# Optimization experiments

Measured on AMD Instinct MI355X. Metric: run time of the kernel, lower is better.

The kernel has to match this reference:

```python
import jax, jax.numpy as jnp
import numpy as np

N_NODES = 100000
N_EDGES = 1600000
NEG_SLOPE = 0.2  # DGL GATConv default leaky_relu slope
BN_EPS = 1e-5


def setup_inputs() -> dict:
    key = jax.random.key(0)
    ks = jax.random.split(key, 10)
    feats = jax.random.normal(ks[0], (N_NODES, 128), dtype=jnp.float32)
    src = jax.random.randint(ks[1], (N_EDGES,), 0, N_NODES, dtype=jnp.int64)
    dst = jax.random.randint(ks[2], (N_EDGES,), 0, N_NODES, dtype=jnp.int64)
    fc_w = jax.random.normal(ks[3], (256, 128), dtype=jnp.float32) * 0.05   # H*D x in_feats
    attn_l = jax.random.normal(ks[4], (4, 64), dtype=jnp.float32) * 0.05
    attn_r = jax.random.normal(ks[5], (4, 64), dtype=jnp.float32) * 0.05
    res_w = jax.random.normal(ks[6], (256, 128), dtype=jnp.float32) * 0.05  # residual projection
    bias = jax.random.normal(ks[7], (4, 64), dtype=jnp.float32) * 0.05
    gamma = jnp.ones((64,), dtype=jnp.float32)
    beta = jnp.zeros((64,), dtype=jnp.float32)
    return {"feats": feats, "src": src, "dst": dst, "fc_w": fc_w,
            "attn_l": attn_l, "attn_r": attn_r, "res_w": res_w,
            "bias": bias, "gamma": gamma, "beta": beta}


def reference(feats, src, dst, fc_w, attn_l, attn_r, res_w, bias, gamma, beta):
    N = feats.shape[0]
    H, D = attn_l.shape
    # projected features [N, H, D] (feat_drop is identity in eval mode)
    h = (feats @ fc_w.T).reshape(N, H, D)
    # per-node attention logits [N, H]
    el = jnp.sum(h * attn_l[None], axis=-1)
    er = jnp.sum(h * attn_r[None], axis=-1)
    # edge logits, leaky relu
    e = el[src] + er[dst]                       # [E, H]
    e = jnp.where(e > 0, e, NEG_SLOPE * e)
    # numerically stable segment softmax over incoming edges of each dst node
    m = jax.ops.segment_max(e, dst, num_segments=N)       # [N, H]
    ex = jnp.exp(e - m[dst])                               # [E, H]
    s = jax.ops.segment_sum(ex, dst, num_segments=N)       # [N, H]
    alpha = ex / s[dst]                                    # [E, H]
    # weighted message aggregation: scatter-add alpha * h_src into dst
    msg = h[src] * alpha[:, :, None]                       # [E, H, D]
    rst = jax.ops.segment_sum(msg, dst, num_segments=N)    # [N, H, D]
    # residual projection + bias + activation (elu)
    res = (feats @ res_w.T).reshape(N, H, D)
    rst = jax.nn.elu(rst + res + bias[None])
    # mean over heads -> [N, D]
    out = rst.mean(axis=1)
    # BatchNorm1d (training stats: biased variance over the node/batch axis)
    mu = out.mean(axis=0)
    var = out.var(axis=0)
    return (out - mu) * jax.lax.rsqrt(var + BN_EPS) * gamma + beta
```

## Files before the change

### kernel.cpp

```cpp
#include <hip/hip_runtime.h>

#define N_NODES 100000
#define N_EDGES 1600000
#define NEG_SLOPE 0.2f
#define BN_EPS 1e-5f

typedef __attribute__((ext_vector_type(8))) short short8;
typedef __attribute__((ext_vector_type(4))) float floatx4;

static const size_t OFF_AB   = 0;
static const size_t OFF_BB   = 25624576;
static const size_t OFF_H    = 25755648;
static const size_t OFF_RES  = 76956672;
static const size_t OFF_EL   = 128156672;
static const size_t OFF_ER   = 129757184;
static const size_t OFF_DEG  = 131357184;
static const size_t OFF_RS   = 131757184;
static const size_t OFF_CUR  = 132157568;
static const size_t OFF_ESRC = 132557568;
static const size_t OFF_BS   = 142157568;
static const size_t OFF_BN   = 142158080;

__device__ __forceinline__ unsigned short f2bf(float x) {
  unsigned int u = __float_as_uint(x);
  unsigned int r = (u + 0x7fffu + ((u >> 16) & 1u)) >> 16;
  return (unsigned short)r;
}
__device__ __forceinline__ float bf2f(unsigned short u) {
  return __uint_as_float(((unsigned int)u) << 16);
}

__global__ __launch_bounds__(256) void k_pre(
    const float* __restrict__ feats, const float* __restrict__ fc_w,
    const float* __restrict__ res_w, const int* __restrict__ dst,
    unsigned short* __restrict__ Ab, unsigned short* __restrict__ Bb,
    int* __restrict__ deg, unsigned short* __restrict__ hbuf,
    float* __restrict__ el)
{
  const int b = blockIdx.x;
  if (b < 6256) {
    int c = b * 256 + threadIdx.x;
    int r = c >> 4, j = c & 15;
    unsigned short v[8];
    if (r < N_NODES) {
      const float* p = feats + (size_t)r * 128 + j * 8;
      float4 a = *(const float4*)p, bb = *(const float4*)(p + 4);
      v[0]=f2bf(a.x); v[1]=f2bf(a.y); v[2]=f2bf(a.z); v[3]=f2bf(a.w);
      v[4]=f2bf(bb.x); v[5]=f2bf(bb.y); v[6]=f2bf(bb.z); v[7]=f2bf(bb.w);
    } else {
      for (int i = 0; i < 8; i++) v[i] = 0;
    }
    size_t idx = (size_t)(r >> 7) * 2048 + ((r >> 4) & 7) * 256 + (j >> 2) * 64
               + (r & 15) + 16 * (j & 3);
    *(short8*)(Ab + idx * 8) = *(short8*)v;
  } else if (b < 12506) {
    int e = (b - 6256) * 256 + threadIdx.x;
    if (e < N_EDGES) atomicAdd(&deg[dst[e]], 1);
  } else if (b < 12538) {
    int c = (b - 12506) * 256 + threadIdx.x;
    int n = c >> 4, j = c & 15;
    const float* W = (n < 256) ? (fc_w + (size_t)n * 128) : (res_w + (size_t)(n - 256) * 128);
    const float* p = W + j * 8;
    float4 a = *(const float4*)p, bb = *(const float4*)(p + 4);
    unsigned short v[8];
    v[0]=f2bf(a.x); v[1]=f2bf(a.y); v[2]=f2bf(a.z); v[3]=f2bf(a.w);
    v[4]=f2bf(bb.x); v[5]=f2bf(bb.y); v[6]=f2bf(bb.z); v[7]=f2bf(bb.w);
    size_t idx = (size_t)(n >> 7) * 2048 + ((n >> 4) & 7) * 256 + (j >> 2) * 64
               + (n & 15) + 16 * (j & 3);
    *(short8*)(Bb + idx * 8) = *(short8*)v;
  } else {
    const int t = threadIdx.x;
    hbuf[(size_t)N_NODES * 256 + t] = 0;
    if (t < 4) el[N_NODES * 4 + t] = -1e30f;
  }
}

__global__ __launch_bounds__(256) void k_mm(
    const unsigned short* __restrict__ Ab, const unsigned short* __restrict__ Bb,
    const float* __restrict__ bias, const float* __restrict__ attn_l,
    const float* __restrict__ attn_r,
    unsigned short* __restrict__ hbuf, unsigned short* __restrict__ resbuf,
    float* __restrict__ el, float* __restrict__ er)
{
  __shared__ unsigned short sA[16384];
  const int tid = threadIdx.x;
  const int w = tid >> 6, L = tid & 63;
  const int blk = blockIdx.x, nb = blockIdx.y;

  {
    const unsigned short* ga = Ab + (size_t)blk * 16384;
    #pragma unroll
    for (int i = 0; i < 8; i++) {
      int off = (i * 256 + w * 64) * 8;
      __builtin_amdgcn_global_load_lds(
          (const __attribute__((address_space(1))) unsigned int*)(ga + off + L * 8),
          (__attribute__((address_space(3))) unsigned int*)(sA + off),
          16, 0, 0);
    }
  }
  const int mh = w & 1, nh = w >> 1;
  floatx4 acc[4][4] = {};
  __syncthreads();

  const unsigned short* gb = Bb + ((size_t)nb * 2048 + nh * 4 * 256) * 8 + L * 8;
  #pragma unroll
  for (int s = 0; s < 4; s++) {
    short8 a[4], b[4];
    #pragma unroll
    for (int t = 0; t < 4; t++)
      a[t] = *(const short8*)(sA + ((mh * 4 + t) * 256 + s * 64 + L) * 8);
    #pragma unroll
    for (int t = 0; t < 4; t++)
      b[t] = *(const short8*)(gb + ((size_t)t * 256 + s * 64) * 8);
    #pragma unroll
    for (int mt = 0; mt < 4; mt++)
      #pragma unroll
      for (int nt = 0; nt < 4; nt++)
        acc[mt][nt] = __builtin_amdgcn_mfma_f32_16x16x32_bf16(a[mt], b[nt], acc[mt][nt], 0, 0, 0);
  }

  const int q = L >> 4, cn = L & 15;
  const int r0 = blk * 128 + mh * 64;
  if (nb < 2) {
    const int head = nb * 2 + nh;
    const int col0 = nb * 128 + nh * 64;
    float al[4], ar[4];
    #pragma unroll
    for (int nt = 0; nt < 4; nt++) {
      al[nt] = attn_l[head * 64 + nt * 16 + cn];
      ar[nt] = attn_r[head * 64 + nt * 16 + cn];
    }
    #pragma unroll
    for (int mt = 0; mt < 4; mt++)
      #pragma unroll
      for (int r = 0; r < 4; r++) {
        const int row = r0 + mt * 16 + q * 4 + r;
        float pl = 0.f, pr = 0.f;
        #pragma unroll
        for (int nt = 0; nt < 4; nt++) {
          pl = fmaf(acc[mt][nt][r], al[nt], pl);
          pr = fmaf(acc[mt][nt][r], ar[nt], pr);
        }
        #pragma unroll
        for (int o = 1; o < 16; o <<= 1) {
          pl += __shfl_xor(pl, o, 64);
          pr += __shfl_xor(pr, o, 64);
        }
        if (row < N_NODES) {
          #pragma unroll
          for (int nt = 0; nt < 4; nt++)
            hbuf[(size_t)row * 256 + col0 + nt * 16 + cn] = f2bf(acc[mt][nt][r]);
          if (cn == 0) {
            el[row * 4 + head] = pl;
            er[row * 4 + head] = pr;
          }
        }
      }
  } else {
    const int rc0 = (nb - 2) * 128 + nh * 64;
    #pragma unroll
    for (int mt = 0; mt < 4; mt++)
      #pragma unroll
      for (int r = 0; r < 4; r++) {
        const int row = r0 + mt * 16 + q * 4 + r;
        if (row < N_NODES)
          #pragma unroll
          for (int nt = 0; nt < 4; nt++) {
            float v = acc[mt][nt][r] + bias[rc0 + nt * 16 + cn];
            resbuf[(size_t)row * 256 + rc0 + nt * 16 + cn] = f2bf(v);
          }
      }
  }
}

__global__ __launch_bounds__(256) void k_scan1(const int* __restrict__ deg,
                                               int* __restrict__ rs, int* __restrict__ bsums)
{
  __shared__ int tmp[256];
  const int t = threadIdx.x;
  const int base = blockIdx.x * 1024 + t * 4;
  int v0 = 0, v1 = 0, v2 = 0, v3 = 0;
  if (base + 0 < N_NODES) v0 = (deg[base + 0] + 3) & ~3;
  if (base + 1 < N_NODES) v1 = (deg[base + 1] + 3) & ~3;
  if (base + 2 < N_NODES) v2 = (deg[base + 2] + 3) & ~3;
  if (base + 3 < N_NODES) v3 = (deg[base + 3] + 3) & ~3;
  const int tsum = v0 + v1 + v2 + v3;
  tmp[t] = tsum;
  __syncthreads();
  for (int o = 1; o < 256; o <<= 1) {
    int x = (t >= o) ? tmp[t - o] : 0;
    __syncthreads();
    tmp[t] += x;
    __syncthreads();
  }
  const int excl = tmp[t] - tsum;
  if (base + 0 < N_NODES) rs[base + 0] = excl;
  if (base + 1 < N_NODES) rs[base + 1] = excl + v0;
  if (base + 2 < N_NODES) rs[base + 2] = excl + v0 + v1;
  if (base + 3 < N_NODES) rs[base + 3] = excl + v0 + v1 + v2;
  if (t == 255) bsums[blockIdx.x] = tmp[t];
}

__global__ __launch_bounds__(256) void k_scan3(int* __restrict__ rs,
                                               const int* __restrict__ bsums,
                                               int* __restrict__ cursor,
                                               const int* __restrict__ deg,
                                               int* __restrict__ esrc)
{
  __shared__ int sb[128];
  const int t = threadIdx.x;
  int raw = 0;
  if (t < 128) { raw = (t < 98) ? bsums[t] : 0; sb[t] = raw; }
  __syncthreads();
  for (int o = 1; o < 128; o <<= 1) {
    int x = (t >= o && t < 128) ? sb[t - o] : 0;
    __syncthreads();
    if (t < 128) sb[t] += x;
    __syncthreads();
  }
  if (t < 128) sb[t] -= raw;
  __syncthreads();
  const int i = blockIdx.x * 256 + t;
  if (i < N_NODES) {
    int v = rs[i] + sb[i >> 10];
    rs[i] = v;
    cursor[i] = v;
    const int d = deg[i];
    const int pd = (d + 3) & ~3;
    for (int j = d; j < pd; j++) esrc[v + j] = N_NODES;
    if (i == N_NODES - 1) rs[N_NODES] = v + pd;
  }
}

__global__ __launch_bounds__(256) void k_scatter(const int* __restrict__ src,
                                                 const int* __restrict__ dst,
                                                 int* __restrict__ cursor,
                                                 int* __restrict__ esrc)
{
  int e = blockIdx.x * 256 + threadIdx.x;
  if (e >= N_EDGES) return;
  int d = dst[e];
  int pos = atomicAdd(&cursor[d], 1);
  esrc[pos] = src[e];
}

#define RFL(x) __builtin_amdgcn_readfirstlane(x)

#define LOADSN4(SN, PP) do { SN = *(const int4*)(esrc + (PP)); } while (0)

#define GATHER4(EV, HV, SN) do { \
  const int g0_ = RFL(SN.x), g1_ = RFL(SN.y), g2_ = RFL(SN.z), g3_ = RFL(SN.w); \
  HV##0 = *(const ushort4*)(hbuf + (size_t)g0_ * 256 + lane4); \
  HV##1 = *(const ushort4*)(hbuf + (size_t)g1_ * 256 + lane4); \
  HV##2 = *(const ushort4*)(hbuf + (size_t)g2_ * 256 + lane4); \
  HV##3 = *(const ushort4*)(hbuf + (size_t)g3_ * 256 + lane4); \
  EV##0 = el[g0_ * 4 + head]; \
  EV##1 = el[g1_ * 4 + head]; \
  EV##2 = el[g2_ * 4 + head]; \
  EV##3 = el[g3_ * 4 + head]; \
} while (0)

#define EDGE1(EVi, HVi) do { \
  float e_ = EVi + ern; \
  e_ = (e_ > 0.f) ? e_ : NEG_SLOPE * e_; \
  const float w_ = __expf(e_); \
  ssum += w_; \
  acc.x = fmaf(w_, bf2f(HVi.x), acc.x); \
  acc.y = fmaf(w_, bf2f(HVi.y), acc.y); \
  acc.z = fmaf(w_, bf2f(HVi.z), acc.z); \
  acc.w = fmaf(w_, bf2f(HVi.w), acc.w); \
} while (0)

#define COMPUTE4(EV, HV) do { \
  EDGE1(EV##0, HV##0); EDGE1(EV##1, HV##1); \
  EDGE1(EV##2, HV##2); EDGE1(EV##3, HV##3); \
} while (0)

#define FIN(ND) do { \
  const float inv_ = (ssum > 0.f) ? (1.0f / ssum) : 0.f; \
  float vx_ = fmaf(acc.x, inv_, bf2f(rv_cur.x)); \
  float vy_ = fmaf(acc.y, inv_, bf2f(rv_cur.y)); \
  float vz_ = fmaf(acc.z, inv_, bf2f(rv_cur.z)); \
  float vw_ = fmaf(acc.w, inv_, bf2f(rv_cur.w)); \
  vx_ = (vx_ > 0.f) ? vx_ : (__expf(vx_) - 1.f); \
  vy_ = (vy_ > 0.f) ? vy_ : (__expf(vy_) - 1.f); \
  vz_ = (vz_ > 0.f) ? vz_ : (__expf(vz_) - 1.f); \
  vw_ = (vw_ > 0.f) ? vw_ : (__expf(vw_) - 1.f); \
  vx_ += __shfl_xor(vx_, 16, 64); vx_ += __shfl_xor(vx_, 32, 64); \
  vy_ += __shfl_xor(vy_, 16, 64); vy_ += __shfl_xor(vy_, 32, 64); \
  vz_ += __shfl_xor(vz_, 16, 64); vz_ += __shfl_xor(vz_, 32, 64); \
  vw_ += __shfl_xor(vw_, 16, 64); vw_ += __shfl_xor(vw_, 32, 64); \
  if (lane < 16) { \
    float4 o_; \
    o_.x = vx_ * 0.25f; o_.y = vy_ * 0.25f; o_.z = vz_ * 0.25f; o_.w = vw_ * 0.25f; \
    *(float4*)(out + (size_t)(ND) * 64 + lane4) = o_; \
  } \
} while (0)

#define BOUNDARY() \
  while (p == nend) { \
    FIN(nu); \
    acc.x = 0.f; acc.y = 0.f; acc.z = 0.f; acc.w = 0.f; ssum = 0.f; \
    nu++; \
    nend = nendN; ern = ernN; rv_cur = rvN; \
    const int f1_ = (nu + 1 < N_NODES) ? (nu + 1) : (N_NODES - 1); \
    const int f2_ = (nu + 2 <= N_NODES) ? (nu + 2) : N_NODES; \
    nendN = RFL(rs[f2_]); \
    ernN = er[f1_ * 4 + head]; \
    rvN = *(const ushort4*)(resbuf + (size_t)f1_ * 256 + lane4); \
  }

__global__ __launch_bounds__(256, 4) void k_agg(
    const unsigned short* __restrict__ hbuf, const unsigned short* __restrict__ resbuf,
    const float* __restrict__ el, const float* __restrict__ er,
    const int* __restrict__ rs, const int* __restrict__ esrc,
    float* __restrict__ out)
{
  const int lane = threadIdx.x & 63;
  const int head = lane >> 4;
  const int lane4 = lane * 4;
  const int wid = blockIdx.x * 4 + (threadIdx.x >> 6);
  const int nW = gridDim.x * 4;

  const int n0 = (int)(((long long)wid * N_NODES) / nW);
  const int n1 = (int)(((long long)(wid + 1) * N_NODES) / nW);
  if (n0 >= n1) return;

  int nu = RFL(n0);
  const int p_end = RFL(rs[n1]);
  int nend = RFL(rs[nu + 1]);
  {
  }
  int f1 = (nu + 1 < N_NODES) ? (nu + 1) : (N_NODES - 1);
  int f2 = (nu + 2 <= N_NODES) ? (nu + 2) : N_NODES;
  int nendN = RFL(rs[f2]);
  float ern  = er[nu * 4 + head];
  float ernN = er[f1 * 4 + head];
  ushort4 rv_cur = *(const ushort4*)(resbuf + (size_t)nu * 256 + lane4);
  ushort4 rvN    = *(const ushort4*)(resbuf + (size_t)f1 * 256 + lane4);

  float4 acc = make_float4(0.f, 0.f, 0.f, 0.f);
  float ssum = 0.f;

  int4 snA, snB, snC, snD;
  float evA0, evA1, evA2, evA3, evB0, evB1, evB2, evB3;
  float evC0, evC1, evC2, evC3, evD0, evD1, evD2, evD3;
  ushort4 hvA0, hvA1, hvA2, hvA3, hvB0, hvB1, hvB2, hvB3;
  ushort4 hvC0, hvC1, hvC2, hvC3, hvD0, hvD1, hvD2, hvD3;

  int p = RFL(rs[nu]);
  if (p      < p_end) { LOADSN4(snA, p);      GATHER4(evA, hvA, snA); }
  if (p + 4  < p_end) { LOADSN4(snB, p + 4);  GATHER4(evB, hvB, snB); }
  if (p + 8  < p_end) { LOADSN4(snC, p + 8);  GATHER4(evC, hvC, snC); }
  if (p + 12 < p_end) { LOADSN4(snD, p + 12); }

  while (p < p_end) {
    if (p + 12 < p_end) GATHER4(evD, hvD, snD);
    if (p + 16 < p_end) LOADSN4(snA, p + 16);
    BOUNDARY();
    COMPUTE4(evA, hvA);
    p += 4; if (p >= p_end) break;
    if (p + 12 < p_end) GATHER4(evA, hvA, snA);
    if (p + 16 < p_end) LOADSN4(snB, p + 16);
    BOUNDARY();
    COMPUTE4(evB, hvB);
    p += 4; if (p >= p_end) break;
    if (p + 12 < p_end) GATHER4(evB, hvB, snB);
    if (p + 16 < p_end) LOADSN4(snC, p + 16);
    BOUNDARY();
    COMPUTE4(evC, hvC);
    p += 4; if (p >= p_end) break;
    if (p + 12 < p_end) GATHER4(evC, hvC, snC);
    if (p + 16 < p_end) LOADSN4(snD, p + 16);
    BOUNDARY();
    COMPUTE4(evD, hvD);
    p += 4;
  }

  while (nu < n1) {
    FIN(nu);
    acc.x = 0.f; acc.y = 0.f; acc.z = 0.f; acc.w = 0.f; ssum = 0.f;
    nu++;
    if (nu < n1) rv_cur = *(const ushort4*)(resbuf + (size_t)nu * 256 + lane4);
  }
}

__global__ __launch_bounds__(256) void k_bn_stats(const float* __restrict__ out,
                                                  float* __restrict__ bn)
{
  const int t = threadIdx.x;
  const int c4 = (t & 15) * 4;
  const int rg = t >> 4;
  float4 s = make_float4(0.f, 0.f, 0.f, 0.f);
  float4 q = make_float4(0.f, 0.f, 0.f, 0.f);
  for (int row = blockIdx.x * 16 + rg; row < N_NODES; row += gridDim.x * 16) {
    float4 v = *(const float4*)(out + (size_t)row * 64 + c4);
    s.x += v.x; s.y += v.y; s.z += v.z; s.w += v.w;
    q.x += v.x * v.x; q.y += v.y * v.y; q.z += v.z * v.z; q.w += v.w * v.w;
  }
  __shared__ float ls[64], lq[64];
  if (t < 64) { ls[t] = 0.f; lq[t] = 0.f; }
  __syncthreads();
  atomicAdd(&ls[c4 + 0], s.x); atomicAdd(&ls[c4 + 1], s.y);
  atomicAdd(&ls[c4 + 2], s.z); atomicAdd(&ls[c4 + 3], s.w);
  atomicAdd(&lq[c4 + 0], q.x); atomicAdd(&lq[c4 + 1], q.y);
  atomicAdd(&lq[c4 + 2], q.z); atomicAdd(&lq[c4 + 3], q.w);
  __syncthreads();
  if (t < 64) {
    atomicAdd(&bn[t], ls[t]);
    atomicAdd(&bn[64 + t], lq[t]);
  }
}

__global__ __launch_bounds__(256) void k_bn_apply(float* __restrict__ out,
                                                  const float* __restrict__ bn,
                                                  const float* __restrict__ gamma,
                                                  const float* __restrict__ beta)
{
  __shared__ float sc[64], sh[64];
  const int t = threadIdx.x;
  if (t < 64) {
    float mean = bn[t] * (1.0f / N_NODES);
    float var = bn[64 + t] * (1.0f / N_NODES) - mean * mean;
    float s = gamma[t] * rsqrtf(var + BN_EPS);
    sc[t] = s;
    sh[t] = beta[t] - mean * s;
  }
  __syncthreads();
  const int i = blockIdx.x * 256 + t;
  if (i >= N_NODES * 16) return;
  const int d0 = (i & 15) * 4;
  float4 v = *(float4*)(out + (size_t)i * 4);
  v.x = fmaf(v.x, sc[d0 + 0], sh[d0 + 0]);
  v.y = fmaf(v.y, sc[d0 + 1], sh[d0 + 1]);
  v.z = fmaf(v.z, sc[d0 + 2], sh[d0 + 2]);
  v.w = fmaf(v.w, sc[d0 + 3], sh[d0 + 3]);
  *(float4*)(out + (size_t)i * 4) = v;
}

extern "C" void kernel_launch(void* const* d_in, const int* in_sizes, int n_in,
                              void* d_out, int out_size, void* d_ws, size_t ws_size,
                              hipStream_t stream)
{
  const float* feats  = (const float*)d_in[0];
  const int*   src    = (const int*)d_in[1];
  const int*   dst    = (const int*)d_in[2];
  const float* fc_w   = (const float*)d_in[3];
  const float* attn_l = (const float*)d_in[4];
  const float* attn_r = (const float*)d_in[5];
  const float* res_w  = (const float*)d_in[6];
  const float* bias   = (const float*)d_in[7];
  const float* gamma  = (const float*)d_in[8];
  const float* beta   = (const float*)d_in[9];

  char* ws = (char*)d_ws;
  unsigned short* Ab     = (unsigned short*)(ws + OFF_AB);
  unsigned short* Bb     = (unsigned short*)(ws + OFF_BB);
  unsigned short* hbuf   = (unsigned short*)(ws + OFF_H);
  unsigned short* resbuf = (unsigned short*)(ws + OFF_RES);
  float* elb    = (float*)(ws + OFF_EL);
  float* erb    = (float*)(ws + OFF_ER);
  int*   deg    = (int*)(ws + OFF_DEG);
  int*   rsb    = (int*)(ws + OFF_RS);
  int*   curb   = (int*)(ws + OFF_CUR);
  int*   esrc   = (int*)(ws + OFF_ESRC);
  int*   bsums  = (int*)(ws + OFF_BS);
  float* bnb    = (float*)(ws + OFF_BN);
  float* outp   = (float*)d_out;

  hipMemsetAsync(deg, 0, N_NODES * sizeof(int), stream);
  hipMemsetAsync(bnb, 0, 128 * sizeof(float), stream);

  k_pre<<<12539, 256, 0, stream>>>(feats, fc_w, res_w, dst, Ab, Bb, deg, hbuf, elb);
  k_mm<<<dim3(782, 4), 256, 0, stream>>>(Ab, Bb, bias, attn_l, attn_r,
                                         hbuf, resbuf, elb, erb);
  k_scan1<<<98, 256, 0, stream>>>(deg, rsb, bsums);
  k_scan3<<<391, 256, 0, stream>>>(rsb, bsums, curb, deg, esrc);
  k_scatter<<<6250, 256, 0, stream>>>(src, dst, curb, esrc);
  k_agg<<<2048, 256, 0, stream>>>(hbuf, resbuf, elb, erb, rsb, esrc, outp);
  k_bn_stats<<<256, 256, 0, stream>>>(outp, bnb);
  k_bn_apply<<<6250, 256, 0, stream>>>(outp, bnb, gamma, beta);
}
```

Baseline: 515.9 us.

## Reuse A tile across two N-blocks in matmul; split edges across half-waves in aggregation

The matmul kernel now loads each A tile into LDS once and loops over two N-blocks, halving the grid's y dimension and the repeated A traffic. The aggregation kernel changes from one wave handling four edges per step with 4 features per lane to each half-wave processing a different edge with 8 features per lane via 16-byte loads. Partial sums are combined across halves with cross-lane shuffles at node boundaries. This is meant to increase per-lane load width and memory-level parallelism, at the cost of extra shuffles, a phase-aligned prologue, and fewer matmul blocks.

```diff
diff --git a/kernel.cpp b/kernel.cpp
--- a/kernel.cpp
+++ b/kernel.cpp
@@ -7,6 +7,7 @@
 
 typedef __attribute__((ext_vector_type(8))) short short8;
 typedef __attribute__((ext_vector_type(4))) float floatx4;
+typedef __attribute__((ext_vector_type(8))) unsigned short u16x8;
 
 static const size_t OFF_AB   = 0;
 static const size_t OFF_BB   = 25624576;
@@ -85,7 +86,7 @@
   __shared__ unsigned short sA[16384];
   const int tid = threadIdx.x;
   const int w = tid >> 6, L = tid & 63;
-  const int blk = blockIdx.x, nb = blockIdx.y;
+  const int blk = blockIdx.x;
 
   {
     const unsigned short* ga = Ab + (size_t)blk * 16384;
@@ -99,77 +100,80 @@
     }
   }
   const int mh = w & 1, nh = w >> 1;
-  floatx4 acc[4][4] = {};
-  __syncthreads();
-
-  const unsigned short* gb = Bb + ((size_t)nb * 2048 + nh * 4 * 256) * 8 + L * 8;
-  #pragma unroll
-  for (int s = 0; s < 4; s++) {
-    short8 a[4], b[4];
+  __syncthreads();
+
+  for (int wb = 0; wb < 2; ++wb) {
+    const int nb = blockIdx.y + wb * 2;
+    floatx4 acc[4][4] = {};
+    const unsigned short* gb = Bb + ((size_t)nb * 2048 + nh * 4 * 256) * 8 + L * 8;
     #pragma unroll
-    for (int t = 0; t < 4; t++)
-      a[t] = *(const short8*)(sA + ((mh * 4 + t) * 256 + s * 64 + L) * 8);
-    #pragma unroll
-    for (int t = 0; t < 4; t++)
-      b[t] = *(const short8*)(gb + ((size_t)t * 256 + s * 64) * 8);
-    #pragma unroll
-    for (int mt = 0; mt < 4; mt++)
+    for (int s = 0; s < 4; s++) {
+      short8 a[4], b[4];
       #pragma unroll
-      for (int nt = 0; nt < 4; nt++)
-        acc[mt][nt] = __builtin_amdgcn_mfma_f32_16x16x32_bf16(a[mt], b[nt], acc[mt][nt], 0, 0, 0);
-  }
-
-  const int q = L >> 4, cn = L & 15;
-  const int r0 = blk * 128 + mh * 64;
-  if (nb < 2) {
-    const int head = nb * 2 + nh;
-    const int col0 = nb * 128 + nh * 64;
-    float al[4], ar[4];
-    #pragma unroll
-    for (int nt = 0; nt < 4; nt++) {
-      al[nt] = attn_l[head * 64 + nt * 16 + cn];
-      ar[nt] = attn_r[head * 64 + nt * 16 + cn];
+      for (int t = 0; t < 4; t++)
+        a[t] = *(const short8*)(sA + ((mh * 4 + t) * 256 + s * 64 + L) * 8);
+      #pragma unroll
+      for (int t = 0; t < 4; t++)
+        b[t] = *(const short8*)(gb + ((size_t)t * 256 + s * 64) * 8);
+      #pragma unroll
+      for (int mt = 0; mt < 4; mt++)
+        #pragma unroll
+        for (int nt = 0; nt < 4; nt++)
+          acc[mt][nt] = __builtin_amdgcn_mfma_f32_16x16x32_bf16(a[mt], b[nt], acc[mt][nt], 0, 0, 0);
     }
-    #pragma unroll
-    for (int mt = 0; mt < 4; mt++)
+
+    const int q = L >> 4, cn = L & 15;
+    const int r0 = blk * 128 + mh * 64;
+    if (nb < 2) {
+      const int head = nb * 2 + nh;
+      const int col0 = nb * 128 + nh * 64;
+      float al[4], ar[4];
       #pragma unroll
-      for (int r = 0; r < 4; r++) {
-        const int row = r0 + mt * 16 + q * 4 + r;
-        float pl = 0.f, pr = 0.f;
+      for (int nt = 0; nt < 4; nt++) {
+        al[nt] = attn_l[head * 64 + nt * 16 + cn];
+        ar[nt] = attn_r[head * 64 + nt * 16 + cn];
+      }
+      #pragma unroll
+      for (int mt = 0; mt < 4; mt++)
         #pragma unroll
-        for (int nt = 0; nt < 4; nt++) {
-          pl = fmaf(acc[mt][nt][r], al[nt], pl);
-          pr = fmaf(acc[mt][nt][r], ar[nt], pr);
-        }
-        #pragma unroll
-        for (int o = 1; o < 16; o <<= 1) {
-          pl += __shfl_xor(pl, o, 64);
-          pr += __shfl_xor(pr, o, 64);
-        }
-        if (row < N_NODES) {
+        for (int r = 0; r < 4; r++) {
+          const int row = r0 + mt * 16 + q * 4 + r;
+          float pl = 0.f, pr = 0.f;
           #pragma unroll
-          for (int nt = 0; nt < 4; nt++)
-            hbuf[(size_t)row * 256 + col0 + nt * 16 + cn] = f2bf(acc[mt][nt][r]);
-          if (cn == 0) {
-            el[row * 4 + head] = pl;
-            er[row * 4 + head] = pr;
+          for (int nt = 0; nt < 4; nt++) {
+            pl = fmaf(acc[mt][nt][r], al[nt], pl);
+            pr = fmaf(acc[mt][nt][r], ar[nt], pr);
+          }
+          #pragma unroll
+          for (int o = 1; o < 16; o <<= 1) {
+            pl += __shfl_xor(pl, o, 64);
+            pr += __shfl_xor(pr, o, 64);
+          }
+          if (row < N_NODES) {
+            #pragma unroll
+            for (int nt = 0; nt < 4; nt++)
+              hbuf[(size_t)row * 256 + col0 + nt * 16 + cn] = f2bf(acc[mt][nt][r]);
+            if (cn == 0) {
+              el[row * 4 + head] = pl;
+              er[row * 4 + head] = pr;
+            }
           }
         }
-      }
-  } else {
-    const int rc0 = (nb - 2) * 128 + nh * 64;
-    #pragma unroll
-    for (int mt = 0; mt < 4; mt++)
+    } else {
+      const int rc0 = (nb - 2) * 128 + nh * 64;
       #pragma unroll
-      for (int r = 0; r < 4; r++) {
-        const int row = r0 + mt * 16 + q * 4 + r;
-        if (row < N_NODES)
-          #pragma unroll
-          for (int nt = 0; nt < 4; nt++) {
-            float v = acc[mt][nt][r] + bias[rc0 + nt * 16 + cn];
-            resbuf[(size_t)row * 256 + rc0 + nt * 16 + cn] = f2bf(v);
-          }
-      }
+      for (int mt = 0; mt < 4; mt++)
+        #pragma unroll
+        for (int r = 0; r < 4; r++) {
+          const int row = r0 + mt * 16 + q * 4 + r;
+          if (row < N_NODES)
+            #pragma unroll
+            for (int nt = 0; nt < 4; nt++) {
+              float v = acc[mt][nt][r] + bias[rc0 + nt * 16 + cn];
+              resbuf[(size_t)row * 256 + rc0 + nt * 16 + cn] = f2bf(v);
+            }
+        }
+    }
   }
 }
 
@@ -246,69 +250,95 @@
 
 #define RFL(x) __builtin_amdgcn_readfirstlane(x)
 
-#define LOADSN4(SN, PP) do { SN = *(const int4*)(esrc + (PP)); } while (0)
-
-#define GATHER4(EV, HV, SN) do { \
-  const int g0_ = RFL(SN.x), g1_ = RFL(SN.y), g2_ = RFL(SN.z), g3_ = RFL(SN.w); \
-  HV##0 = *(const ushort4*)(hbuf + (size_t)g0_ * 256 + lane4); \
-  HV##1 = *(const ushort4*)(hbuf + (size_t)g1_ * 256 + lane4); \
-  HV##2 = *(const ushort4*)(hbuf + (size_t)g2_ * 256 + lane4); \
-  HV##3 = *(const ushort4*)(hbuf + (size_t)g3_ * 256 + lane4); \
-  EV##0 = el[g0_ * 4 + head]; \
-  EV##1 = el[g1_ * 4 + head]; \
-  EV##2 = el[g2_ * 4 + head]; \
-  EV##3 = el[g3_ * 4 + head]; \
+#define GATHER(X) do { \
+  const int s_ = (lane & 32) ? sn##X.y : sn##X.x; \
+  hv##X = *(const u16x8*)(hbuf + (size_t)s_ * 256 + li8); \
+  ev##X = el[s_ * 4 + head]; \
 } while (0)
 
-#define EDGE1(EVi, HVi) do { \
-  float e_ = EVi + ern; \
-  e_ = (e_ > 0.f) ? e_ : NEG_SLOPE * e_; \
+#define PRO(X, B) do { \
+  if ((B) < p_end) { sn##X = *(const int2*)(esrc + (B)); GATHER(X); } \
+} while (0)
+
+#define COMPUTE(X) do { \
+  float e_ = ev##X + ern; \
+  e_ = fmaxf(e_, NEG_SLOPE * e_); \
   const float w_ = __expf(e_); \
   ssum += w_; \
-  acc.x = fmaf(w_, bf2f(HVi.x), acc.x); \
-  acc.y = fmaf(w_, bf2f(HVi.y), acc.y); \
-  acc.z = fmaf(w_, bf2f(HVi.z), acc.z); \
-  acc.w = fmaf(w_, bf2f(HVi.w), acc.w); \
+  accA.x = fmaf(w_, bf2f(hv##X[0]), accA.x); \
+  accA.y = fmaf(w_, bf2f(hv##X[1]), accA.y); \
+  accA.z = fmaf(w_, bf2f(hv##X[2]), accA.z); \
+  accA.w = fmaf(w_, bf2f(hv##X[3]), accA.w); \
+  accB.x = fmaf(w_, bf2f(hv##X[4]), accB.x); \
+  accB.y = fmaf(w_, bf2f(hv##X[5]), accB.y); \
+  accB.z = fmaf(w_, bf2f(hv##X[6]), accB.z); \
+  accB.w = fmaf(w_, bf2f(hv##X[7]), accB.w); \
 } while (0)
 
-#define COMPUTE4(EV, HV) do { \
-  EDGE1(EV##0, HV##0); EDGE1(EV##1, HV##1); \
-  EDGE1(EV##2, HV##2); EDGE1(EV##3, HV##3); \
-} while (0)
-
 #define FIN(ND) do { \
-  const float inv_ = (ssum > 0.f) ? (1.0f / ssum) : 0.f; \
-  float vx_ = fmaf(acc.x, inv_, bf2f(rv_cur.x)); \
-  float vy_ = fmaf(acc.y, inv_, bf2f(rv_cur.y)); \
-  float vz_ = fmaf(acc.z, inv_, bf2f(rv_cur.z)); \
-  float vw_ = fmaf(acc.w, inv_, bf2f(rv_cur.w)); \
-  vx_ = (vx_ > 0.f) ? vx_ : (__expf(vx_) - 1.f); \
-  vy_ = (vy_ > 0.f) ? vy_ : (__expf(vy_) - 1.f); \
-  vz_ = (vz_ > 0.f) ? vz_ : (__expf(vz_) - 1.f); \
-  vw_ = (vw_ > 0.f) ? vw_ : (__expf(vw_) - 1.f); \
-  vx_ += __shfl_xor(vx_, 16, 64); vx_ += __shfl_xor(vx_, 32, 64); \
-  vy_ += __shfl_xor(vy_, 16, 64); vy_ += __shfl_xor(vy_, 32, 64); \
-  vz_ += __shfl_xor(vz_, 16, 64); vz_ += __shfl_xor(vz_, 32, 64); \
-  vw_ += __shfl_xor(vw_, 16, 64); vw_ += __shfl_xor(vw_, 32, 64); \
-  if (lane < 16) { \
-    float4 o_; \
-    o_.x = vx_ * 0.25f; o_.y = vy_ * 0.25f; o_.z = vz_ * 0.25f; o_.w = vw_ * 0.25f; \
-    *(float4*)(out + (size_t)(ND) * 64 + lane4) = o_; \
+  float st_ = ssum + __shfl_xor(ssum, 32, 64); \
+  float a0_ = accA.x + __shfl_xor(accA.x, 32, 64); \
+  float a1_ = accA.y + __shfl_xor(accA.y, 32, 64); \
+  float a2_ = accA.z + __shfl_xor(accA.z, 32, 64); \
+  float a3_ = accA.w + __shfl_xor(accA.w, 32, 64); \
+  float a4_ = accB.x + __shfl_xor(accB.x, 32, 64); \
+  float a5_ = accB.y + __shfl_xor(accB.y, 32, 64); \
+  float a6_ = accB.z + __shfl_xor(accB.z, 32, 64); \
+  float a7_ = accB.w + __shfl_xor(accB.w, 32, 64); \
+  const float inv_ = (st_ > 0.f) ? (1.0f / st_) : 0.f; \
+  a0_ = fmaf(a0_, inv_, bf2f(rv_cur[0])); \
+  a1_ = fmaf(a1_, inv_, bf2f(rv_cur[1])); \
+  a2_ = fmaf(a2_, inv_, bf2f(rv_cur[2])); \
+  a3_ = fmaf(a3_, inv_, bf2f(rv_cur[3])); \
+  a4_ = fmaf(a4_, inv_, bf2f(rv_cur[4])); \
+  a5_ = fmaf(a5_, inv_, bf2f(rv_cur[5])); \
+  a6_ = fmaf(a6_, inv_, bf2f(rv_cur[6])); \
+  a7_ = fmaf(a7_, inv_, bf2f(rv_cur[7])); \
+  a0_ = (a0_ > 0.f) ? a0_ : (__expf(a0_) - 1.f); \
+  a1_ = (a1_ > 0.f) ? a1_ : (__expf(a1_) - 1.f); \
+  a2_ = (a2_ > 0.f) ? a2_ : (__expf(a2_) - 1.f); \
+  a3_ = (a3_ > 0.f) ? a3_ : (__expf(a3_) - 1.f); \
+  a4_ = (a4_ > 0.f) ? a4_ : (__expf(a4_) - 1.f); \
+  a5_ = (a5_ > 0.f) ? a5_ : (__expf(a5_) - 1.f); \
+  a6_ = (a6_ > 0.f) ? a6_ : (__expf(a6_) - 1.f); \
+  a7_ = (a7_ > 0.f) ? a7_ : (__expf(a7_) - 1.f); \
+  a0_ += __shfl_xor(a0_, 8, 64);  a0_ += __shfl_xor(a0_, 16, 64); \
+  a1_ += __shfl_xor(a1_, 8, 64);  a1_ += __shfl_xor(a1_, 16, 64); \
+  a2_ += __shfl_xor(a2_, 8, 64);  a2_ += __shfl_xor(a2_, 16, 64); \
+  a3_ += __shfl_xor(a3_, 8, 64);  a3_ += __shfl_xor(a3_, 16, 64); \
+  a4_ += __shfl_xor(a4_, 8, 64);  a4_ += __shfl_xor(a4_, 16, 64); \
+  a5_ += __shfl_xor(a5_, 8, 64);  a5_ += __shfl_xor(a5_, 16, 64); \
+  a6_ += __shfl_xor(a6_, 8, 64);  a6_ += __shfl_xor(a6_, 16, 64); \
+  a7_ += __shfl_xor(a7_, 8, 64);  a7_ += __shfl_xor(a7_, 16, 64); \
+  if (lane < 8) { \
+    float4 o1_, o2_; \
+    o1_.x = a0_ * 0.25f; o1_.y = a1_ * 0.25f; o1_.z = a2_ * 0.25f; o1_.w = a3_ * 0.25f; \
+    o2_.x = a4_ * 0.25f; o2_.y = a5_ * 0.25f; o2_.z = a6_ * 0.25f; o2_.w = a7_ * 0.25f; \
+    *(float4*)(out + (size_t)(ND) * 64 + li8) = o1_; \
+    *(float4*)(out + (size_t)(ND) * 64 + li8 + 4) = o2_; \
   } \
 } while (0)
 
 #define BOUNDARY() \
   while (p == nend) { \
     FIN(nu); \
-    acc.x = 0.f; acc.y = 0.f; acc.z = 0.f; acc.w = 0.f; ssum = 0.f; \
+    accA.x=0.f; accA.y=0.f; accA.z=0.f; accA.w=0.f; \
+    accB.x=0.f; accB.y=0.f; accB.z=0.f; accB.w=0.f; ssum = 0.f; \
     nu++; \
     nend = nendN; ern = ernN; rv_cur = rvN; \
     const int f1_ = (nu + 1 < N_NODES) ? (nu + 1) : (N_NODES - 1); \
     const int f2_ = (nu + 2 <= N_NODES) ? (nu + 2) : N_NODES; \
     nendN = RFL(rs[f2_]); \
     ernN = er[f1_ * 4 + head]; \
-    rvN = *(const ushort4*)(resbuf + (size_t)f1_ * 256 + lane4); \
-  }
+    rvN = *(const u16x8*)(resbuf + (size_t)f1_ * 256 + li8); \
+  }
+
+#define STEP(CUR, NXT) do { \
+  if (p + 6 < p_end) GATHER(NXT); \
+  if (p + 8 < p_end) sn##CUR = *(const int2*)(esrc + p + 8); \
+  BOUNDARY(); \
+  COMPUTE(CUR); \
+} while (0)
 
 __global__ __launch_bounds__(256, 4) void k_agg(
     const unsigned short* __restrict__ hbuf, const unsigned short* __restrict__ resbuf,
@@ -317,8 +347,9 @@
     float* __restrict__ out)
 {
   const int lane = threadIdx.x & 63;
-  const int head = lane >> 4;
-  const int lane4 = lane * 4;
+  const int li = lane & 31;
+  const int head = li >> 3;
+  const int li8 = li * 8;
   const int wid = blockIdx.x * 4 + (threadIdx.x >> 6);
   const int nW = gridDim.x * 4;
 
@@ -329,59 +360,49 @@
   int nu = RFL(n0);
   const int p_end = RFL(rs[n1]);
   int nend = RFL(rs[nu + 1]);
-  {
-  }
   int f1 = (nu + 1 < N_NODES) ? (nu + 1) : (N_NODES - 1);
   int f2 = (nu + 2 <= N_NODES) ? (nu + 2) : N_NODES;
   int nendN = RFL(rs[f2]);
   float ern  = er[nu * 4 + head];
   float ernN = er[f1 * 4 + head];
-  ushort4 rv_cur = *(const ushort4*)(resbuf + (size_t)nu * 256 + lane4);
-  ushort4 rvN    = *(const ushort4*)(resbuf + (size_t)f1 * 256 + lane4);
-
-  float4 acc = make_float4(0.f, 0.f, 0.f, 0.f);
+  u16x8 rv_cur = *(const u16x8*)(resbuf + (size_t)nu * 256 + li8);
+  u16x8 rvN    = *(const u16x8*)(resbuf + (size_t)f1 * 256 + li8);
+
+  float4 accA = make_float4(0.f, 0.f, 0.f, 0.f);
+  float4 accB = make_float4(0.f, 0.f, 0.f, 0.f);
   float ssum = 0.f;
 
-  int4 snA, snB, snC, snD;
-  float evA0, evA1, evA2, evA3, evB0, evB1, evB2, evB3;
-  float evC0, evC1, evC2, evC3, evD0, evD1, evD2, evD3;
-  ushort4 hvA0, hvA1, hvA2, hvA3, hvB0, hvB1, hvB2, hvB3;
-  ushort4 hvC0, hvC1, hvC2, hvC3, hvD0, hvD1, hvD2, hvD3;
+  int2 snA, snB, snC, snD;
+  float evA, evB, evC, evD;
+  u16x8 hvA, hvB, hvC, hvD;
 
   int p = RFL(rs[nu]);
-  if (p      < p_end) { LOADSN4(snA, p);      GATHER4(evA, hvA, snA); }
-  if (p + 4  < p_end) { LOADSN4(snB, p + 4);  GATHER4(evB, hvB, snB); }
-  if (p + 8  < p_end) { LOADSN4(snC, p + 8);  GATHER4(evC, hvC, snC); }
-  if (p + 12 < p_end) { LOADSN4(snD, p + 12); }
-
+  const int ph = (p >> 1) & 3;
+  if (ph == 0) {
+    PRO(A, p); PRO(B, p + 2); PRO(C, p + 4);
+    if (p + 6 < p_end) snD = *(const int2*)(esrc + p + 6);
+  } else {
+    PRO(C, p); PRO(D, p + 2); PRO(A, p + 4);
+    if (p + 6 < p_end) snB = *(const int2*)(esrc + p + 6);
+  }
+
+  if (ph == 2 && p < p_end) {
+    STEP(C, B); p += 2;
+    if (p < p_end) { STEP(D, C); p += 2; }
+  }
   while (p < p_end) {
-    if (p + 12 < p_end) GATHER4(evD, hvD, snD);
-    if (p + 16 < p_end) LOADSN4(snA, p + 16);
-    BOUNDARY();
-    COMPUTE4(evA, hvA);
-    p += 4; if (p >= p_end) break;
-    if (p + 12 < p_end) GATHER4(evA, hvA, snA);
-    if (p + 16 < p_end) LOADSN4(snB, p + 16);
-    BOUNDARY();
-    COMPUTE4(evB, hvB);
-    p += 4; if (p >= p_end) break;
-    if (p + 12 < p_end) GATHER4(evB, hvB, snB);
-    if (p + 16 < p_end) LOADSN4(snC, p + 16);
-    BOUNDARY();
-    COMPUTE4(evC, hvC);
-    p += 4; if (p >= p_end) break;
-    if (p + 12 < p_end) GATHER4(evC, hvC, snC);
-    if (p + 16 < p_end) LOADSN4(snD, p + 16);
-    BOUNDARY();
-    COMPUTE4(evD, hvD);
-    p += 4;
+    STEP(A, D); p += 2; if (p >= p_end) break;
+    STEP(B, A); p += 2; if (p >= p_end) break;
+    STEP(C, B); p += 2; if (p >= p_end) break;
+    STEP(D, C); p += 2;
   }
 
   while (nu < n1) {
     FIN(nu);
-    acc.x = 0.f; acc.y = 0.f; acc.z = 0.f; acc.w = 0.f; ssum = 0.f;
+    accA.x=0.f; accA.y=0.f; accA.z=0.f; accA.w=0.f;
+    accB.x=0.f; accB.y=0.f; accB.z=0.f; accB.w=0.f; ssum = 0.f;
     nu++;
-    if (nu < n1) rv_cur = *(const ushort4*)(resbuf + (size_t)nu * 256 + lane4);
+    if (nu < n1) rv_cur = *(const u16x8*)(resbuf + (size_t)nu * 256 + li8);
   }
 }
 
@@ -472,7 +493,7 @@
   hipMemsetAsync(bnb, 0, 128 * sizeof(float), stream);
 
   k_pre<<<12539, 256, 0, stream>>>(feats, fc_w, res_w, dst, Ab, Bb, deg, hbuf, elb);
-  k_mm<<<dim3(782, 4), 256, 0, stream>>>(Ab, Bb, bias, attn_l, attn_r,
+  k_mm<<<dim3(782, 2), 256, 0, stream>>>(Ab, Bb, bias, attn_l, attn_r,
                                          hbuf, resbuf, elb, erb);
   k_scan1<<<98, 256, 0, stream>>>(deg, rsb, bsums);
   k_scan3<<<391, 256, 0, stream>>>(rsb, bsums, curb, deg, esrc);
```

Measured after the change: 526.9 us. 2.1% more time.
